# Performance work log

Measured on AMD Instinct MI355X. Metric: run time of the kernel, lower is better.

Reference implementation:

```python
import jax, jax.numpy as jnp
import numpy as np

N = 50000        # nodes
E_RAND = 800000  # random edges; self-loops appended (A_hat = A + I)
IN = 512         # in_size
OUT = 64         # out_size per head
H = 8            # num_heads
NEG_SLOPE = 0.01 # torch F.leaky_relu default


def setup_inputs() -> dict:
    key = jax.random.key(0)
    k0, k1, k2, k3, k4, k5 = jax.random.split(key, 6)
    X = jax.random.normal(k0, (N, IN), jnp.float32)
    W = jax.random.normal(k1, (OUT * H, IN), jnp.float32) * (1.0 / np.sqrt(IN))
    b = jnp.zeros((OUT * H,), jnp.float32)
    a_l = jax.random.normal(k2, (1, OUT, H), jnp.float32) * 0.1
    a_r = jax.random.normal(k3, (1, OUT, H), jnp.float32) * 0.1
    # edges: random graph plus self-loops so every row segment is non-empty
    row = jnp.concatenate([jax.random.randint(k4, (E_RAND,), 0, N, jnp.int32),
                           jnp.arange(N, dtype=jnp.int32)])
    col = jnp.concatenate([jax.random.randint(k5, (E_RAND,), 0, N, jnp.int32),
                           jnp.arange(N, dtype=jnp.int32)])
    return {"X": X, "W": W, "b": b, "a_l": a_l, "a_r": a_r, "row": row, "col": col}


def reference(X, W, b, a_l, a_r, row, col):
    # dropout p=0.0 -> identity (eval-mode equivalent)
    Z = (X @ W.T + b).reshape(N, OUT, H)              # [N, OUT, H]
    e_l = jnp.sum(Z * a_l, axis=1)                    # [N, H]
    e_r = jnp.sum(Z * a_r, axis=1)                    # [N, H]
    e = jax.nn.leaky_relu(e_l[row] + e_r[col], NEG_SLOPE)  # [E, H]
    # segment softmax over edges grouped by destination row
    m = jax.ops.segment_max(e, row, num_segments=N)   # [N, H]
    ex = jnp.exp(e - m[row])                          # [E, H]
    denom = jax.ops.segment_sum(ex, row, num_segments=N)  # [N, H]
    a = ex / denom[row]                               # [E, H]
    # bspmm: out[i,:,h] = sum_{e: row[e]=i} a[e,h] * Z[col[e],:,h]
    msg = a[:, None, :] * Z[col]                      # [E, OUT, H]
    out = jax.ops.segment_sum(msg, row, num_segments=N)   # [N, OUT, H]
    return out
```

## Files before the change

### kernel.cpp

```cpp
#include <hip/hip_runtime.h>
#include <hip/hip_fp16.h>

#define IN_F 512
#define OH   512
#define NH   8

typedef _Float16 half_t;
typedef __attribute__((ext_vector_type(8))) _Float16 f16x8;
typedef __attribute__((ext_vector_type(4))) float    f32x4;

#define GLOBAL_AS const __attribute__((address_space(1))) void
#define LDS_AS    __attribute__((address_space(3))) void

__device__ static inline void gload_lds16(const void* g, void* l) {
  __builtin_amdgcn_global_load_lds((GLOBAL_AS*)g, (LDS_AS*)l, 16, 0, 0);
}

__global__ __launch_bounds__(256) void k_castW(const float* __restrict__ W,
                                               half_t* __restrict__ Wh, int n) {
  int i = (blockIdx.x * 256 + threadIdx.x) * 8;
  if (i >= n) return;
  float4 a = *(const float4*)(W + i);
  float4 b = *(const float4*)(W + i + 4);
  f16x8 h;
  h[0] = (half_t)a.x; h[1] = (half_t)a.y; h[2] = (half_t)a.z; h[3] = (half_t)a.w;
  h[4] = (half_t)b.x; h[5] = (half_t)b.y; h[6] = (half_t)b.z; h[7] = (half_t)b.w;
  *(f16x8*)(Wh + i) = h;
}

__global__ __launch_bounds__(256) void k_gemm16_v3(const float* __restrict__ X,
                                                   const half_t* __restrict__ Wh,
                                                   const float* __restrict__ bias,
                                                   const float* __restrict__ al,
                                                   const float* __restrict__ ar,
                                                   half_t* __restrict__ Zh,
                                                   float* __restrict__ el,
                                                   float* __restrict__ er,
                                                   int N, int nwg) {
  __shared__ float  As[2][128][32];
  __shared__ half_t Bs[2][128][32];
  const int tid  = threadIdx.x;
  const int lane = tid & 63;
  const int wid  = tid >> 6;
  const int wr = wid >> 1, wc = wid & 1;

  int orig = blockIdx.x;
  int xcd = orig & 7;
  int q = nwg >> 3, r = nwg & 7;
  int start = (xcd < r) ? xcd * (q + 1) : r * (q + 1) + (xcd - r) * q;
  int work = start + (orig >> 3);
  const int n0 = (work >> 2) * 128;
  const int j0 = (work & 3) * 128;

  f32x4 acc[4][4] = {};

  const int rl = lane & 15;
  const int hi16 = lane >> 4;
  const int kg = hi16 * 8;

  int a_row[4], a_gsg[4];
#pragma unroll
  for (int c = 0; c < 4; c++) {
    int off = wid * 4096 + c * 1024 + lane * 16;
    int row = off >> 7;
    int sg  = (off >> 4) & 7;
    a_row[c] = row;
    a_gsg[c] = sg ^ (row & 7);
  }
  int b_row[2], b_colh[2];
#pragma unroll
  for (int c = 0; c < 2; c++) {
    int off = wid * 2048 + c * 1024 + lane * 16;
    b_row[c]  = off >> 6;
    b_colh[c] = (off >> 1) & 31;
  }

#define STAGE(BUF, KT)                                                         \
  do {                                                                         \
    _Pragma("unroll")                                                          \
    for (int c = 0; c < 4; c++) {                                              \
      int an = n0 + a_row[c]; if (an >= N) an = N - 1;                         \
      const float* g = X + (size_t)an * IN_F + (KT) + a_gsg[c] * 4;            \
      gload_lds16(g, (char*)&As[BUF][0][0] + wid * 4096 + c * 1024);           \
    }                                                                          \
    _Pragma("unroll")                                                          \
    for (int c = 0; c < 2; c++) {                                              \
      const half_t* g = Wh + (size_t)(j0 + b_row[c]) * IN_F + (KT) + b_colh[c];\
      gload_lds16(g, (char*)&Bs[BUF][0][0] + wid * 2048 + c * 1024);           \
    }                                                                          \
  } while (0)

  STAGE(0, 0);

#pragma unroll
  for (int ki = 0; ki < IN_F / 32; ki++) {
    const int cur = ki & 1;
    if (ki < IN_F / 32 - 1) {
      STAGE(cur ^ 1, (ki + 1) * 32);
      asm volatile("s_waitcnt vmcnt(6)" ::: "memory");
    } else {
      asm volatile("s_waitcnt vmcnt(0)" ::: "memory");
    }
    __builtin_amdgcn_s_barrier();

    f16x8 af[4], bf[4];
#pragma unroll
    for (int m = 0; m < 4; m++) {
      int row = wr * 64 + m * 16 + rl;
      int r7 = row & 7;
      int ga = hi16 * 2;
      const char* base = (const char*)&As[cur][row][0];
      f32x4 lo = *(const f32x4*)(base + ((ga ^ r7) << 4));
      f32x4 hi = *(const f32x4*)(base + (((ga + 1) ^ r7) << 4));
      f16x8 a;
#pragma unroll
      for (int u = 0; u < 4; u++) { a[u] = (half_t)lo[u]; a[u + 4] = (half_t)hi[u]; }
      af[m] = a;
    }
#pragma unroll
    for (int n = 0; n < 4; n++)
      bf[n] = *(const f16x8*)&Bs[cur][wc * 64 + n * 16 + rl][kg];

#pragma unroll
    for (int m = 0; m < 4; m++)
#pragma unroll
      for (int n = 0; n < 4; n++)
        acc[m][n] = __builtin_amdgcn_mfma_f32_16x16x32_f16(af[m], bf[n], acc[m][n], 0, 0, 0);

    __builtin_amdgcn_s_barrier();
  }
#undef STAGE

  float partl[4][4], partr[4][4];
#pragma unroll
  for (int m = 0; m < 4; m++)
#pragma unroll
    for (int qq = 0; qq < 4; qq++) { partl[m][qq] = 0.f; partr[m][qq] = 0.f; }

#pragma unroll
  for (int n = 0; n < 4; n++) {
    int j = j0 + wc * 64 + n * 16 + rl;
    float bv = bias[j];
    float av = al[j];
    float rv = ar[j];
#pragma unroll
    for (int m = 0; m < 4; m++) {
      int rbase = n0 + wr * 64 + m * 16 + hi16 * 4;
#pragma unroll
      for (int qq = 0; qq < 4; qq++) {
        float v = acc[m][n][qq] + bv;
        int nrow = rbase + qq;
        if (nrow < N) Zh[(size_t)nrow * OH + j] = (half_t)v;
        partl[m][qq] = fmaf(v, av, partl[m][qq]);
        partr[m][qq] = fmaf(v, rv, partr[m][qq]);
      }
    }
  }
  const int h = rl & 7;
#pragma unroll
  for (int m = 0; m < 4; m++) {
#pragma unroll
    for (int qq = 0; qq < 4; qq++) {
      float pl = partl[m][qq], pr = partr[m][qq];
      pl += __shfl_xor(pl, 8);
      pr += __shfl_xor(pr, 8);
      if (rl < 8) {
        int nrow = n0 + wr * 64 + m * 16 + hi16 * 4 + qq;
        if (nrow < N) {
          atomicAdd(&el[(size_t)nrow * NH + h], pl);
          atomicAdd(&er[(size_t)nrow * NH + h], pr);
        }
      }
    }
  }
}

__global__ void k_hist(const int* __restrict__ row, int* __restrict__ deg, int E) {
  int e = blockIdx.x * blockDim.x + threadIdx.x;
  if (e < E) atomicAdd(&deg[row[e]], 1);
}

#define SCAN_B 1024
__global__ __launch_bounds__(SCAN_B) void k_scan1(const int* __restrict__ deg,
                                                  int* __restrict__ off,
                                                  int* __restrict__ sums, int N) {
  __shared__ int s[SCAN_B];
  int tid = threadIdx.x;
  int g = blockIdx.x * SCAN_B + tid;
  int v = (g < N) ? deg[g] : 0;
  s[tid] = v;
  __syncthreads();
  for (int o = 1; o < SCAN_B; o <<= 1) {
    int t = (tid >= o) ? s[tid - o] : 0;
    __syncthreads();
    s[tid] += t;
    __syncthreads();
  }
  if (g < N) off[g] = s[tid] - v;
  if (tid == SCAN_B - 1) sums[blockIdx.x] = s[tid];
}

__global__ __launch_bounds__(SCAN_B) void k_scan3(int* __restrict__ off,
                                                  int* __restrict__ cursor,
                                                  const int* __restrict__ sums,
                                                  int nb, int N, int E) {
  __shared__ int sboff;
  int tid = threadIdx.x;
  if (tid < 64) {
    int v = (tid < nb && tid < (int)blockIdx.x) ? sums[tid] : 0;
#pragma unroll
    for (int s = 1; s < 64; s <<= 1) v += __shfl_xor(v, s);
    if (tid == 0) sboff = v;
  }
  __syncthreads();
  int g = blockIdx.x * SCAN_B + tid;
  if (g < N) {
    int v = off[g] + sboff;
    off[g] = v;
    cursor[g] = v;
  }
  if (g == 0) off[N] = E;
}

__global__ void k_fill(const int* __restrict__ row, const int* __restrict__ col,
                       int* __restrict__ cursor, int* __restrict__ colS, int E) {
  int e = blockIdx.x * blockDim.x + threadIdx.x;
  if (e < E) {
    int r = row[e];
    int p = atomicAdd(&cursor[r], 1);
    colS[p] = col[e];
  }
}

__global__ __launch_bounds__(256) void k_attagg(const half_t* __restrict__ Zh,
                                                const float* __restrict__ el,
                                                const float* __restrict__ er,
                                                const int* __restrict__ off,
                                                const int* __restrict__ colS,
                                                float* __restrict__ out, int N) {
  __shared__ float wts[4][64][NH];
  __shared__ int   cls[4][64];
  int wid = threadIdx.x >> 6, lane = threadIdx.x & 63;
  int i = blockIdx.x * 4 + wid;
  if (i >= N) return;
  int s = off[i], t = off[i + 1];
  int deg = t - s;

  float eli[8];
  {
    const float4* e4 = (const float4*)(el + (size_t)i * NH);
    float4 a = e4[0], b = e4[1];
    eli[0] = a.x; eli[1] = a.y; eli[2] = a.z; eli[3] = a.w;
    eli[4] = b.x; eli[5] = b.y; eli[6] = b.z; eli[7] = b.w;
  }

  float m[8], ehs[8];
  int csave = 0;
#pragma unroll
  for (int h = 0; h < 8; h++) m[h] = -1e30f;
  for (int p = s + lane; p < t; p += 64) {
    int c = colS[p];
    csave = c;
    const float4* e4 = (const float4*)(er + (size_t)c * NH);
    float4 ea = e4[0], eb = e4[1];
    float ev[8] = {ea.x, ea.y, ea.z, ea.w, eb.x, eb.y, eb.z, eb.w};
#pragma unroll
    for (int h = 0; h < 8; h++) {
      float eh = eli[h] + ev[h];
      eh = (eh > 0.f) ? eh : 0.01f * eh;
      ehs[h] = eh;
      m[h] = fmaxf(m[h], eh);
    }
  }
#pragma unroll
  for (int st = 1; st < 64; st <<= 1)
#pragma unroll
    for (int h = 0; h < 8; h++) m[h] = fmaxf(m[h], __shfl_xor(m[h], st));

  float acc[8], den[8];
#pragma unroll
  for (int h = 0; h < 8; h++) { acc[h] = 0.f; den[h] = 0.f; }

  for (int base = s; base < t; base += 64) {
    int p = base + lane;
    if (p < t) {
      int c;
      float eh[8];
      if (deg <= 64) {
        c = csave;
#pragma unroll
        for (int h = 0; h < 8; h++) eh[h] = ehs[h];
      } else {
        c = colS[p];
        const float4* e4 = (const float4*)(er + (size_t)c * NH);
        float4 ea = e4[0], eb = e4[1];
        float ev[8] = {ea.x, ea.y, ea.z, ea.w, eb.x, eb.y, eb.z, eb.w};
#pragma unroll
        for (int h = 0; h < 8; h++) {
          float e2 = eli[h] + ev[h];
          eh[h] = (e2 > 0.f) ? e2 : 0.01f * e2;
        }
      }
      cls[wid][lane] = c;
#pragma unroll
      for (int h = 0; h < 8; h++) {
        float pr = __expf(eh[h] - m[h]);
        den[h] += pr;
        wts[wid][lane][h] = pr;
      }
    }
    int cnt = t - base; if (cnt > 64) cnt = 64;

    int e = 0;
    for (; e + 4 <= cnt; e += 4) {
      int c0 = cls[wid][e + 0], c1 = cls[wid][e + 1];
      int c2 = cls[wid][e + 2], c3 = cls[wid][e + 3];
      f16x8 z0 = *(const f16x8*)(Zh + (size_t)c0 * OH + lane * 8);
      f16x8 z1 = *(const f16x8*)(Zh + (size_t)c1 * OH + lane * 8);
      f16x8 z2 = *(const f16x8*)(Zh + (size_t)c2 * OH + lane * 8);
      f16x8 z3 = *(const f16x8*)(Zh + (size_t)c3 * OH + lane * 8);
      const float* w0 = &wts[wid][e + 0][0];
      const float* w1 = &wts[wid][e + 1][0];
      const float* w2 = &wts[wid][e + 2][0];
      const float* w3 = &wts[wid][e + 3][0];
#pragma unroll
      for (int h = 0; h < 8; h++) {
        acc[h] = fmaf(w0[h], (float)z0[h], acc[h]);
        acc[h] = fmaf(w1[h], (float)z1[h], acc[h]);
        acc[h] = fmaf(w2[h], (float)z2[h], acc[h]);
        acc[h] = fmaf(w3[h], (float)z3[h], acc[h]);
      }
    }
    for (; e < cnt; e++) {
      int c = cls[wid][e];
      f16x8 z = *(const f16x8*)(Zh + (size_t)c * OH + lane * 8);
      const float* w = &wts[wid][e][0];
#pragma unroll
      for (int h = 0; h < 8; h++) acc[h] = fmaf(w[h], (float)z[h], acc[h]);
    }
  }

#pragma unroll
  for (int st = 1; st < 64; st <<= 1)
#pragma unroll
    for (int h = 0; h < 8; h++) den[h] += __shfl_xor(den[h], st);

  float4 o0 = make_float4(acc[0] / den[0], acc[1] / den[1],
                          acc[2] / den[2], acc[3] / den[3]);
  float4 o1 = make_float4(acc[4] / den[4], acc[5] / den[5],
                          acc[6] / den[6], acc[7] / den[7]);
  *(float4*)(out + (size_t)i * OH + lane * 8)     = o0;
  *(float4*)(out + (size_t)i * OH + lane * 8 + 4) = o1;
}

extern "C" void kernel_launch(void* const* d_in, const int* in_sizes, int n_in,
                              void* d_out, int out_size, void* d_ws, size_t ws_size,
                              hipStream_t stream) {
  const float* X    = (const float*)d_in[0];
  const float* W    = (const float*)d_in[1];
  const float* bias = (const float*)d_in[2];
  const float* a_l  = (const float*)d_in[3];
  const float* a_r  = (const float*)d_in[4];
  const int*   row  = (const int*)d_in[5];
  const int*   col  = (const int*)d_in[6];
  float* out = (float*)d_out;

  const int N = in_sizes[0] / IN_F;
  const int E = in_sizes[5];
  const int nWe = OH * IN_F;

  auto align_up = [](size_t v) { return (v + 255) & ~(size_t)255; };
  char* p = (char*)d_ws;
  half_t* Wh    = (half_t*)p; p += align_up((size_t)nWe * 2);
  half_t* Zh    = (half_t*)p; p += align_up((size_t)N * OH * 2);
  float* el     = (float*)p;  p += (size_t)N * NH * 4;
  float* er     = (float*)p;  p += align_up((size_t)N * NH * 4);
  int*   deg    = (int*)p;    p += align_up((size_t)N * 4);
  int*   off    = (int*)p;    p += align_up((size_t)(N + 1) * 4);
  int*   cursor = (int*)p;    p += align_up((size_t)N * 4);
  int*   sums   = (int*)p;    p += align_up((size_t)64 * 4);
  int*   colS   = (int*)p;    p += align_up((size_t)E * 4);
  (void)ws_size; (void)n_in; (void)out_size;

  const int nb = (N + SCAN_B - 1) / SCAN_B;

  hipMemsetAsync(deg, 0, (size_t)N * 4, stream);
  hipMemsetAsync(el, 0, (size_t)2 * N * NH * 4, stream);

  hipLaunchKernelGGL(k_castW, dim3((nWe / 8 + 255) / 256), dim3(256), 0, stream,
                     W, Wh, nWe);

  const int nwg = ((N + 127) / 128) * 4;
  hipLaunchKernelGGL(k_gemm16_v3, dim3(nwg), dim3(256), 0, stream,
                     X, Wh, bias, a_l, a_r, Zh, el, er, N, nwg);

  hipLaunchKernelGGL(k_hist, dim3((E + 255) / 256), dim3(256), 0, stream, row, deg, E);
  hipLaunchKernelGGL(k_scan1, dim3(nb), dim3(SCAN_B), 0, stream, deg, off, sums, N);
  hipLaunchKernelGGL(k_scan3, dim3(nb), dim3(SCAN_B), 0, stream,
                     off, cursor, sums, nb, N, E);
  hipLaunchKernelGGL(k_fill, dim3((E + 255) / 256), dim3(256), 0, stream,
                     row, col, cursor, colS, E);

  hipLaunchKernelGGL(k_attagg, dim3((N + 3) / 4), dim3(256), 0, stream,
                     Zh, el, er, off, colS, out, N);
}
```

Measured before the change: 338.6 us.

## Load GEMM operands directly from global memory and use nontemporal loads/stores in aggregation

The projection GEMM drops its double-buffered LDS staging with async global-to-LDS loads and barriers. Each wave now reads its A rows (fp32 X) and B rows (fp16 W) straight from global memory into registers before the MFMAs. Operands are no longer shared across waves through LDS, so each X and W element is fetched by several waves and relies on cache hits, with no explicit prefetch overlap. Separately, the attention-aggregation kernel reads colS with nontemporal loads and writes the output with nontemporal stores to reduce cache pollution.

```diff
diff --git a/kernel.cpp b/kernel.cpp
--- a/kernel.cpp
+++ b/kernel.cpp
@@ -8,13 +8,6 @@
 typedef _Float16 half_t;
 typedef __attribute__((ext_vector_type(8))) _Float16 f16x8;
 typedef __attribute__((ext_vector_type(4))) float    f32x4;
-
-#define GLOBAL_AS const __attribute__((address_space(1))) void
-#define LDS_AS    __attribute__((address_space(3))) void
-
-__device__ static inline void gload_lds16(const void* g, void* l) {
-  __builtin_amdgcn_global_load_lds((GLOBAL_AS*)g, (LDS_AS*)l, 16, 0, 0);
-}
 
 __global__ __launch_bounds__(256) void k_castW(const float* __restrict__ W,
                                                half_t* __restrict__ Wh, int n) {
@@ -28,17 +21,15 @@
   *(f16x8*)(Wh + i) = h;
 }
 
-__global__ __launch_bounds__(256) void k_gemm16_v3(const float* __restrict__ X,
-                                                   const half_t* __restrict__ Wh,
-                                                   const float* __restrict__ bias,
-                                                   const float* __restrict__ al,
-                                                   const float* __restrict__ ar,
-                                                   half_t* __restrict__ Zh,
-                                                   float* __restrict__ el,
-                                                   float* __restrict__ er,
-                                                   int N, int nwg) {
-  __shared__ float  As[2][128][32];
-  __shared__ half_t Bs[2][128][32];
+__global__ __launch_bounds__(256) void k_gemm_direct(const float* __restrict__ X,
+                                                     const half_t* __restrict__ Wh,
+                                                     const float* __restrict__ bias,
+                                                     const float* __restrict__ al,
+                                                     const float* __restrict__ ar,
+                                                     half_t* __restrict__ Zh,
+                                                     float* __restrict__ el,
+                                                     float* __restrict__ er,
+                                                     int N, int nwg) {
   const int tid  = threadIdx.x;
   const int lane = tid & 63;
   const int wid  = tid >> 6;
@@ -52,84 +43,41 @@
   const int n0 = (work >> 2) * 128;
   const int j0 = (work & 3) * 128;
 
-  f32x4 acc[4][4] = {};
-
   const int rl = lane & 15;
   const int hi16 = lane >> 4;
   const int kg = hi16 * 8;
 
-  int a_row[4], a_gsg[4];
-#pragma unroll
-  for (int c = 0; c < 4; c++) {
-    int off = wid * 4096 + c * 1024 + lane * 16;
-    int row = off >> 7;
-    int sg  = (off >> 4) & 7;
-    a_row[c] = row;
-    a_gsg[c] = sg ^ (row & 7);
-  }
-  int b_row[2], b_colh[2];
-#pragma unroll
-  for (int c = 0; c < 2; c++) {
-    int off = wid * 2048 + c * 1024 + lane * 16;
-    b_row[c]  = off >> 6;
-    b_colh[c] = (off >> 1) & 31;
-  }
-
-#define STAGE(BUF, KT)                                                         \
-  do {                                                                         \
-    _Pragma("unroll")                                                          \
-    for (int c = 0; c < 4; c++) {                                              \
-      int an = n0 + a_row[c]; if (an >= N) an = N - 1;                         \
-      const float* g = X + (size_t)an * IN_F + (KT) + a_gsg[c] * 4;            \
-      gload_lds16(g, (char*)&As[BUF][0][0] + wid * 4096 + c * 1024);           \
-    }                                                                          \
-    _Pragma("unroll")                                                          \
-    for (int c = 0; c < 2; c++) {                                              \
-      const half_t* g = Wh + (size_t)(j0 + b_row[c]) * IN_F + (KT) + b_colh[c];\
-      gload_lds16(g, (char*)&Bs[BUF][0][0] + wid * 2048 + c * 1024);           \
-    }                                                                          \
-  } while (0)
-
-  STAGE(0, 0);
-
-#pragma unroll
-  for (int ki = 0; ki < IN_F / 32; ki++) {
-    const int cur = ki & 1;
-    if (ki < IN_F / 32 - 1) {
-      STAGE(cur ^ 1, (ki + 1) * 32);
-      asm volatile("s_waitcnt vmcnt(6)" ::: "memory");
-    } else {
-      asm volatile("s_waitcnt vmcnt(0)" ::: "memory");
-    }
-    __builtin_amdgcn_s_barrier();
-
+  f32x4 acc[4][4] = {};
+
+  const float*  aptr[4];
+  const half_t* bptr[4];
+#pragma unroll
+  for (int m = 0; m < 4; m++) {
+    int rA = n0 + wr * 64 + m * 16 + rl; if (rA >= N) rA = N - 1;
+    aptr[m] = X + (size_t)rA * IN_F + kg;
+    int rB = j0 + wc * 64 + m * 16 + rl;
+    bptr[m] = Wh + (size_t)rB * IN_F + kg;
+  }
+
+#pragma unroll 4
+  for (int kt = 0; kt < IN_F; kt += 32) {
     f16x8 af[4], bf[4];
 #pragma unroll
     for (int m = 0; m < 4; m++) {
-      int row = wr * 64 + m * 16 + rl;
-      int r7 = row & 7;
-      int ga = hi16 * 2;
-      const char* base = (const char*)&As[cur][row][0];
-      f32x4 lo = *(const f32x4*)(base + ((ga ^ r7) << 4));
-      f32x4 hi = *(const f32x4*)(base + (((ga + 1) ^ r7) << 4));
+      f32x4 lo = *(const f32x4*)(aptr[m] + kt);
+      f32x4 hi = *(const f32x4*)(aptr[m] + kt + 4);
       f16x8 a;
 #pragma unroll
       for (int u = 0; u < 4; u++) { a[u] = (half_t)lo[u]; a[u + 4] = (half_t)hi[u]; }
       af[m] = a;
-    }
-#pragma unroll
-    for (int n = 0; n < 4; n++)
-      bf[n] = *(const f16x8*)&Bs[cur][wc * 64 + n * 16 + rl][kg];
-
+      bf[m] = *(const f16x8*)(bptr[m] + kt);
+    }
 #pragma unroll
     for (int m = 0; m < 4; m++)
 #pragma unroll
       for (int n = 0; n < 4; n++)
         acc[m][n] = __builtin_amdgcn_mfma_f32_16x16x32_f16(af[m], bf[n], acc[m][n], 0, 0, 0);
-
-    __builtin_amdgcn_s_barrier();
-  }
-#undef STAGE
+  }
 
   float partl[4][4], partr[4][4];
 #pragma unroll
@@ -259,7 +207,7 @@
 #pragma unroll
   for (int h = 0; h < 8; h++) m[h] = -1e30f;
   for (int p = s + lane; p < t; p += 64) {
-    int c = colS[p];
+    int c = __builtin_nontemporal_load(&colS[p]);
     csave = c;
     const float4* e4 = (const float4*)(er + (size_t)c * NH);
     float4 ea = e4[0], eb = e4[1];
@@ -291,7 +239,7 @@
 #pragma unroll
         for (int h = 0; h < 8; h++) eh[h] = ehs[h];
       } else {
-        c = colS[p];
+        c = __builtin_nontemporal_load(&colS[p]);
         const float4* e4 = (const float4*)(er + (size_t)c * NH);
         float4 ea = e4[0], eb = e4[1];
         float ev[8] = {ea.x, ea.y, ea.z, ea.w, eb.x, eb.y, eb.z, eb.w};
@@ -345,12 +293,13 @@
 #pragma unroll
     for (int h = 0; h < 8; h++) den[h] += __shfl_xor(den[h], st);
 
-  float4 o0 = make_float4(acc[0] / den[0], acc[1] / den[1],
-                          acc[2] / den[2], acc[3] / den[3]);
-  float4 o1 = make_float4(acc[4] / den[4], acc[5] / den[5],
-                          acc[6] / den[6], acc[7] / den[7]);
-  *(float4*)(out + (size_t)i * OH + lane * 8)     = o0;
-  *(float4*)(out + (size_t)i * OH + lane * 8 + 4) = o1;
+  f32x4 o0, o1;
+  o0[0] = acc[0] / den[0]; o0[1] = acc[1] / den[1];
+  o0[2] = acc[2] / den[2]; o0[3] = acc[3] / den[3];
+  o1[0] = acc[4] / den[4]; o1[1] = acc[5] / den[5];
+  o1[2] = acc[6] / den[6]; o1[3] = acc[7] / den[7];
+  __builtin_nontemporal_store(o0, (f32x4*)(out + (size_t)i * OH + lane * 8));
+  __builtin_nontemporal_store(o1, (f32x4*)(out + (size_t)i * OH + lane * 8 + 4));
 }
 
 extern "C" void kernel_launch(void* const* d_in, const int* in_sizes, int n_in,
@@ -391,7 +340,7 @@
                      W, Wh, nWe);
 
   const int nwg = ((N + 127) / 128) * 4;
-  hipLaunchKernelGGL(k_gemm16_v3, dim3(nwg), dim3(256), 0, stream,
+  hipLaunchKernelGGL(k_gemm_direct, dim3(nwg), dim3(256), 0, stream,
                      X, Wh, bias, a_l, a_r, Zh, el, er, N, nwg);
 
   hipLaunchKernelGGL(k_hist, dim3((E + 255) / 256), dim3(256), 0, stream, row, deg, E);
```

Result: slower. 440.7 us (+30.2%).
